# Optimization experiments

Hardware: AMD Instinct MI355X
Metric: run time of the kernel (lower is better)

The kernel has to match this reference:

```python
import jax, jax.numpy as jnp
import numpy as np

DIM = 512
DEPTH = 4
E = 2 ** DEPTH          # 16 experts
HID = 4 * DIM           # mult = 4
B, S = 8, 4096


def setup_inputs() -> dict:
    key = jax.random.key(0)
    ks = jax.random.split(key, 7)
    sc_in = 1.0 / np.sqrt(DIM)
    sc_hid = 1.0 / np.sqrt(HID)
    return {
        "x": jax.random.normal(ks[0], (B, S, DIM), jnp.float32),
        "Wr": jax.random.normal(ks[1], (E - 1, DIM), jnp.float32) * sc_in,
        "br": jax.random.normal(ks[2], (E - 1,), jnp.float32) * 0.01,
        "W1": jax.random.normal(ks[3], (E, DIM, HID), jnp.float32) * sc_in,
        "b1": jax.random.normal(ks[4], (E, HID), jnp.float32) * 0.01,
        "W2": jax.random.normal(ks[5], (E, HID, DIM), jnp.float32) * sc_hid,
        "b2": jax.random.normal(ks[6], (E, DIM), jnp.float32) * 0.01,
    }


def _fff_forward(x, Wr, br, W1, b1, W2, b2):
    Bb, Ss, D = x.shape
    E_ = W1.shape[0]
    depth = int(np.log2(E_))
    xf = x.reshape(-1, D)                      # [N, D]
    N = xf.shape[0]

    # Hard binary-tree routing (inference path of the torch module).
    leaf = jnp.zeros((N,), jnp.int32)
    for d in range(depth):
        off = 2 ** d - 1
        cnt = 2 ** d
        # logits for all routers at this tree level: [N, cnt]
        logits = xf @ Wr[off:off + cnt].T + br[off:off + cnt]
        sel = jnp.take_along_axis(logits, leaf[:, None], axis=1)[:, 0]
        leaf = leaf * 2 + (sel > 0).astype(jnp.int32)

    onehot = jax.nn.one_hot(leaf, E_, dtype=xf.dtype)  # [N, E]

    # Dense weighted-sum dispatch: scan over the (small, fixed) expert axis,
    # accumulating masked expert outputs. Peak extra memory is one [N, HID]
    # activation at a time.
    def body(acc, params):
        w1, bb1, w2, bb2, m = params            # m: [N]
        h = jax.nn.gelu(xf @ w1 + bb1, approximate=False)  # exact GELU (torch nn.GELU)
        y = h @ w2 + bb2
        return acc + m[:, None] * y, None

    out, _ = jax.lax.scan(body, jnp.zeros_like(xf), (W1, b1, W2, b2, onehot.T))
    return out.reshape(Bb, Ss, D)


def reference(x, Wr, br, W1, b1, W2, b2):
    return _fff_forward(x, Wr, br, W1, b1, W2, b2)
```

## Files before the change

kernel.cpp:

```cpp
#include <hip/hip_runtime.h>
#include <math.h>

#define NTOK   32768
#define DMODEL 512
#define HIDDEN 2048
#define NEXP   16
#define TM     256
#define MAXT   144
#define PADN   (MAXT * TM)
#define CPAD   16

typedef short bf16x8 __attribute__((ext_vector_type(8)));
typedef float f32x4  __attribute__((ext_vector_type(4)));

__device__ __forceinline__ short f2bf(float f) {
  union { float f; unsigned int u; } v; v.f = f;
  unsigned int r = v.u + 0x7FFFu + ((v.u >> 16) & 1u);
  return (short)(r >> 16);
}

__device__ __forceinline__ void gload_lds16(const void* g, void* l) {
  __builtin_amdgcn_global_load_lds(
      (const __attribute__((address_space(1))) void*)g,
      (__attribute__((address_space(3))) void*)l, 16, 0, 0);
}

__device__ __forceinline__ float gelu_f(float v) {
  const float u = v * (0.7978845608f + 0.0356774081f * v * v);
  const float au = fabsf(u);
  const float z = __expf(-2.0f * au);
  float T = (1.0f - z) / (1.0f + z);
  T = copysignf(T, u);
  return 0.5f * v * (1.0f + T);
}

__global__ void init_kernel(int* counts, int* cursors) {
  counts[threadIdx.x] = 0; cursors[threadIdx.x] = 0;
}

__global__ __launch_bounds__(256) void route_kernel(
    const float* __restrict__ x, const float* __restrict__ Wr,
    const float* __restrict__ br, short* __restrict__ xb,
    int* __restrict__ leafArr) {
  const int w = threadIdx.x >> 6, l = threadIdx.x & 63;
  const int tok = blockIdx.x * 4 + w;
  const float4* xr = (const float4*)(x + (size_t)tok * DMODEL);
  float4 a0 = xr[l * 2], a1 = xr[l * 2 + 1];

  union { bf16x8 v; short s[8]; } u;
  u.s[0] = f2bf(a0.x); u.s[1] = f2bf(a0.y); u.s[2] = f2bf(a0.z); u.s[3] = f2bf(a0.w);
  u.s[4] = f2bf(a1.x); u.s[5] = f2bf(a1.y); u.s[6] = f2bf(a1.z); u.s[7] = f2bf(a1.w);
  *((bf16x8*)(xb + (size_t)tok * DMODEL) + l) = u.v;

  int leaf = 0;
  for (int d = 0; d < 4; ++d) {
    const int node = (1 << d) - 1 + leaf;
    const float4* wr4 = (const float4*)(Wr + (size_t)node * DMODEL);
    float4 b0 = wr4[l * 2], b1v = wr4[l * 2 + 1];
    double s = (double)a0.x * (double)b0.x + (double)a0.y * (double)b0.y +
               (double)a0.z * (double)b0.z + (double)a0.w * (double)b0.w +
               (double)a1.x * (double)b1v.x + (double)a1.y * (double)b1v.y +
               (double)a1.z * (double)b1v.z + (double)a1.w * (double)b1v.w;
    for (int off = 32; off; off >>= 1) s += __shfl_xor(s, off);
    double sel = s + (double)br[node];
    leaf = leaf * 2 + (sel > 0.0 ? 1 : 0);
  }
  if (l == 0) leafArr[tok] = leaf;
}

__global__ __launch_bounds__(256) void count_kernel(
    const int* __restrict__ leafArr, int* __restrict__ counts,
    int* __restrict__ idx) {
  __shared__ int lcnt[NEXP];
  const int tid = threadIdx.x;
  if (tid < NEXP) lcnt[tid] = 0;
  __syncthreads();
  const int tok = blockIdx.x * 256 + tid;
  atomicAdd(&lcnt[leafArr[tok]], 1);
  __syncthreads();
  if (tid < NEXP && lcnt[tid]) atomicAdd(&counts[tid * CPAD], lcnt[tid]);
  for (int i = blockIdx.x * 256 + tid; i < PADN; i += gridDim.x * 256) idx[i] = 0;
}

__global__ void scan_kernel(const int* __restrict__ counts, int* poff, int* ntiles,
                            int* texp, int* tval) {
  if (threadIdx.x == 0) {
    int po = 0, nt = 0;
    for (int e = 0; e < NEXP; ++e) {
      poff[e] = po;
      const int c = counts[e * CPAD];
      const int t = (c + TM - 1) >> 8;
      for (int i = 0; i < t; ++i) {
        texp[nt] = e;
        int v = c - i * TM; if (v > TM) v = TM;
        tval[nt] = v;
        ++nt;
      }
      po += t << 8;
    }
    poff[NEXP] = po;
    *ntiles = nt;
  }
}

__global__ __launch_bounds__(256) void scatter_kernel(
    const int* __restrict__ leafArr, const int* __restrict__ poff,
    int* cursors, int* __restrict__ idx) {
  __shared__ int lcnt[NEXP], lbase[NEXP];
  const int tid = threadIdx.x;
  if (tid < NEXP) lcnt[tid] = 0;
  __syncthreads();
  const int tok = blockIdx.x * 256 + tid;
  const int e = leafArr[tok];
  const int r = atomicAdd(&lcnt[e], 1);
  __syncthreads();
  if (tid < NEXP) lbase[tid] = lcnt[tid] ? atomicAdd(&cursors[tid * CPAD], lcnt[tid]) : 0;
  __syncthreads();
  idx[poff[e] + lbase[e] + r] = tok;
}

__global__ void tconv_kernel(const float* __restrict__ src, short* __restrict__ dst,
                             int R, int C) {
  __shared__ float tile[32][33];
  const int tx = threadIdx.x, ty = threadIdx.y;
  const int c0 = blockIdx.x * 32, r0 = blockIdx.y * 32;
  const size_t eoff = (size_t)blockIdx.z * R * C;
  for (int i = 0; i < 4; ++i)
    tile[ty + i * 8][tx] = src[eoff + (size_t)(r0 + ty + i * 8) * C + c0 + tx];
  __syncthreads();
  for (int i = 0; i < 4; ++i)
    dst[eoff + (size_t)(c0 + ty + i * 8) * R + r0 + tx] = f2bf(tile[tx][ty + i * 8]);
}


#define STA(pn, ko)                                                            \
  { _Pragma("unroll") for (int j = 0; j < 4; ++j)                              \
      gload_lds16(aSrc[j] + (ko), lds + ((pn) << 14) + j * 4096 + w * 512); }

#define STB(pn, ko)                                                            \
  { _Pragma("unroll") for (int j = 0; j < 4; ++j)                              \
      gload_lds16(bSrc[j] + (ko), lds + 32768 + ((pn) << 14) + j * 4096 + w * 512); }

#define PHASE(mh, ki, STAGE, POST)                                             \
  {                                                                            \
    bf16x8 af[4];                                                              \
    const int sw_ = ((((ki) << 2) + q) ^ (cc & 7)) << 3;                       \
    _Pragma("unroll")                                                          \
    for (int m2 = 0; m2 < 4; ++m2)                                             \
      af[m2] = *(const bf16x8*)(Ab + (wr + ((mh) * 4 + m2) * 16 + cc) * 64 + sw_); \
    if ((mh) == 0) {                                                           \
      _Pragma("unroll")                                                        \
      for (int ni = 0; ni < 4; ++ni)                                           \
        bfv[ni] = *(const bf16x8*)(Bb + (wc + ni * 16 + cc) * 64 + sw_);       \
    }                                                                          \
    STAGE                                                                      \
    __builtin_amdgcn_s_barrier();                                              \
    __builtin_amdgcn_s_setprio(1);                                             \
    _Pragma("unroll")                                                          \
    for (int m2 = 0; m2 < 4; ++m2) {                                           \
      _Pragma("unroll")                                                        \
      for (int ni = 0; ni < 4; ++ni)                                           \
        acc[(mh) * 4 + m2][ni] = __builtin_amdgcn_mfma_f32_16x16x32_bf16(      \
            af[m2], bfv[ni], acc[(mh) * 4 + m2][ni], 0, 0, 0);                 \
    }                                                                          \
    __builtin_amdgcn_s_setprio(0);                                             \
    POST                                                                       \
    __builtin_amdgcn_s_barrier();                                              \
  }

__global__ __launch_bounds__(512, 2) void gemm1_kernel(
    const short* __restrict__ Xb, const short* __restrict__ W1T,
    const float* __restrict__ b1, const int* __restrict__ idx,
    const int* __restrict__ texp, const int* __restrict__ ntiles,
    short* __restrict__ H, int g0) {
  __shared__ short lds[65536];
  const int nb = gridDim.x, bid = blockIdx.x;
  int swz = bid;
  if ((nb & 7) == 0) { const int cpx = nb >> 3; swz = (bid & 7) * cpx + (bid >> 3); }
  const int lt = swz >> 3, cb = swz & 7;
  const int t = g0 + lt;
  if (t >= *ntiles) return;
  const int e = texp[t];
  const int c0 = cb * 256;

  const int tid = threadIdx.x, w = tid >> 6, lane = tid & 63;
  const int q = lane >> 4, cc = lane & 15;
  const int wr = (w >> 2) * 128, wc = (w & 3) * 64;
  const int srow = lane >> 3;
  const int skel = ((lane & 7) ^ srow) * 8;

  const short* aSrc[4]; const short* bSrc[4];
#pragma unroll
  for (int j = 0; j < 4; ++j) {
    const int r = j * 64 + w * 8 + srow;
    const int gt = idx[t * TM + r];
    aSrc[j] = Xb + (size_t)gt * DMODEL + skel;
    bSrc[j] = W1T + ((size_t)e * HIDDEN + c0 + r) * DMODEL + skel;
  }

  f32x4 acc[8][4];
  const f32x4 zero = {0.f, 0.f, 0.f, 0.f};
#pragma unroll
  for (int mi = 0; mi < 8; ++mi)
#pragma unroll
    for (int ni = 0; ni < 4; ++ni) acc[mi][ni] = zero;
  bf16x8 bfv[4];

  STA(0, 0) STB(0, 0)
  asm volatile("s_waitcnt vmcnt(0)" ::: "memory");
  __builtin_amdgcn_s_barrier();

  for (int kt = 0; kt < DMODEL / 64; ++kt) {
    const short* Ab = lds + ((kt & 1) << 14);
    const short* Bb = lds + 32768 + ((kt & 1) << 14);
    const int pn = (kt & 1) ^ 1;
    const int ko = (kt + 1) << 6;
    const bool pre = kt < DMODEL / 64 - 1;
    PHASE(0, 0, if (pre) STA(pn, ko), )
    PHASE(1, 0, if (pre) STB(pn, ko), )
    PHASE(0, 1, , )
    PHASE(1, 1, , asm volatile("s_waitcnt vmcnt(0)" ::: "memory");)
  }

  short* Cs = lds;
#pragma unroll
  for (int ni = 0; ni < 4; ++ni) {
    const int col = wc + ni * 16 + cc;
    const float bv = b1[e * HIDDEN + c0 + col];
#pragma unroll
    for (int mi = 0; mi < 8; ++mi) {
#pragma unroll
      for (int r = 0; r < 4; ++r) {
        const int row = wr + mi * 16 + q * 4 + r;
        const float v = gelu_f(acc[mi][ni][r] + bv);
        Cs[row * 256 + ((((col >> 3) ^ (row & 15)) << 3) | (col & 7))] = f2bf(v);
      }
    }
  }
  __syncthreads();
#pragma unroll
  for (int it = 0; it < 16; ++it) {
    const int lin = tid + it * 512;
    const int row = lin >> 5;
    const int s = lin & 31;
    const bf16x8 vv = *(const bf16x8*)(Cs + row * 256 + s * 8);
    const int ch = s ^ (row & 15);
    *(bf16x8*)(H + ((size_t)lt * TM + row) * HIDDEN + c0 + (ch << 3)) = vv;
  }
}

__global__ __launch_bounds__(512, 2) void gemm2_kernel(
    const short* __restrict__ H, const short* __restrict__ W2T,
    const float* __restrict__ b2, const int* __restrict__ idx,
    const int* __restrict__ texp, const int* __restrict__ tval,
    const int* __restrict__ ntiles, float* __restrict__ out, int g0) {
  __shared__ short lds[65536];
  const int nb = gridDim.x, bid = blockIdx.x;
  int swz = bid;
  if ((nb & 7) == 0) { const int cpx = nb >> 3; swz = (bid & 7) * cpx + (bid >> 3); }
  const int lt = swz >> 1, cb = swz & 1;
  const int t = g0 + lt;
  if (t >= *ntiles) return;
  const int e = texp[t];
  const int c0 = cb * 256;

  const int tid = threadIdx.x, w = tid >> 6, lane = tid & 63;
  const int q = lane >> 4, cc = lane & 15;
  const int wr = (w >> 2) * 128, wc = (w & 3) * 64;
  const int srow = lane >> 3;
  const int skel = ((lane & 7) ^ srow) * 8;

  const short* aSrc[4]; const short* bSrc[4];
#pragma unroll
  for (int j = 0; j < 4; ++j) {
    const int r = j * 64 + w * 8 + srow;
    aSrc[j] = H + ((size_t)lt * TM + r) * HIDDEN + skel;
    bSrc[j] = W2T + ((size_t)e * DMODEL + c0 + r) * HIDDEN + skel;
  }

  f32x4 acc[8][4];
  const f32x4 zero = {0.f, 0.f, 0.f, 0.f};
#pragma unroll
  for (int mi = 0; mi < 8; ++mi)
#pragma unroll
    for (int ni = 0; ni < 4; ++ni) acc[mi][ni] = zero;
  bf16x8 bfv[4];

  STA(0, 0) STB(0, 0)
  asm volatile("s_waitcnt vmcnt(0)" ::: "memory");
  __builtin_amdgcn_s_barrier();

  for (int kt = 0; kt < HIDDEN / 64; ++kt) {
    const short* Ab = lds + ((kt & 1) << 14);
    const short* Bb = lds + 32768 + ((kt & 1) << 14);
    const int pn = (kt & 1) ^ 1;
    const int ko = (kt + 1) << 6;
    const bool pre = kt < HIDDEN / 64 - 1;
    PHASE(0, 0, if (pre) STA(pn, ko), )
    PHASE(1, 0, if (pre) STB(pn, ko), )
    PHASE(0, 1, , )
    PHASE(1, 1, , asm volatile("s_waitcnt vmcnt(0)" ::: "memory");)
  }

  const int nv = tval[t];
#pragma unroll
  for (int ni = 0; ni < 4; ++ni) {
    const int col = c0 + wc + ni * 16 + cc;
    const float bv = b2[e * DMODEL + col];
#pragma unroll
    for (int mi = 0; mi < 8; ++mi) {
#pragma unroll
      for (int r = 0; r < 4; ++r) {
        const int row = wr + mi * 16 + q * 4 + r;
        if (row < nv) {
          const int tok = idx[t * TM + row];
          out[(size_t)tok * DMODEL + col] = acc[mi][ni][r] + bv;
        }
      }
    }
  }
}

extern "C" void kernel_launch(void* const* d_in, const int* in_sizes, int n_in,
                              void* d_out, int out_size, void* d_ws, size_t ws_size,
                              hipStream_t stream) {
  (void)in_sizes; (void)n_in; (void)out_size;
  const float* x  = (const float*)d_in[0];
  const float* Wr = (const float*)d_in[1];
  const float* br = (const float*)d_in[2];
  const float* W1 = (const float*)d_in[3];
  const float* b1 = (const float*)d_in[4];
  const float* W2 = (const float*)d_in[5];
  const float* b2 = (const float*)d_in[6];
  float* out = (float*)d_out;
  char* ws = (char*)d_ws;

  int* counts  = (int*)(ws + 0);
  int* cursors = (int*)(ws + 1024);
  int* poff    = (int*)(ws + 2048);
  int* ntiles  = (int*)(ws + 2304);
  int* texp    = (int*)(ws + 4096);
  int* tval    = (int*)(ws + 8192);
  int* leafA   = (int*)(ws + 16384);
  int* idx     = (int*)(ws + 16384 + 131072);

  const size_t MB32 = 33554432ull;
  short* Xb  = (short*)(ws + (1ull << 20));
  short* W1T = (short*)(ws + (1ull << 20) + MB32);
  short* W2T = (short*)(ws + (1ull << 20) + 2 * MB32);
  short* Hb  = (short*)(ws + (1ull << 20) + 3 * MB32);
  const size_t o_h = (1ull << 20) + 3 * MB32;
  const size_t perTile = (size_t)TM * HIDDEN * sizeof(short);

  int TPG = MAXT;
  if (ws_size < o_h + (size_t)MAXT * perTile) {
    size_t avail = ws_size > o_h ? ws_size - o_h : 0;
    TPG = (int)(avail / perTile);
    TPG &= ~3;
    if (TPG < 4) TPG = 4;
  }
  const int ngroups = (MAXT + TPG - 1) / TPG;

  hipLaunchKernelGGL(init_kernel,    dim3(1),          dim3(256),   0, stream, counts, cursors);
  hipLaunchKernelGGL(route_kernel,   dim3(NTOK / 4),   dim3(256),   0, stream, x, Wr, br, Xb, leafA);
  hipLaunchKernelGGL(count_kernel,   dim3(NTOK / 256), dim3(256),   0, stream, leafA, counts, idx);
  hipLaunchKernelGGL(scan_kernel,    dim3(1),          dim3(64),    0, stream, counts, poff, ntiles, texp, tval);
  hipLaunchKernelGGL(scatter_kernel, dim3(NTOK / 256), dim3(256),   0, stream, leafA, poff, cursors, idx);
  hipLaunchKernelGGL(tconv_kernel,   dim3(64, 16, 16), dim3(32, 8), 0, stream, W1, W1T, DMODEL, HIDDEN);
  hipLaunchKernelGGL(tconv_kernel,   dim3(16, 64, 16), dim3(32, 8), 0, stream, W2, W2T, HIDDEN, DMODEL);

  for (int g = 0; g < ngroups; ++g) {
    hipLaunchKernelGGL(gemm1_kernel, dim3(TPG * 8), dim3(512), 0, stream,
                       Xb, W1T, b1, idx, texp, ntiles, Hb, g * TPG);
    hipLaunchKernelGGL(gemm2_kernel, dim3(TPG * 2), dim3(512), 0, stream,
                       Hb, W2T, b2, idx, texp, tval, ntiles, out, g * TPG);
  }
}
```

Before: 572.6 us.

## Prefetch weight tiles two k-steps ahead with partial vmcnt waits

Replaces the one-stage prefetch loop in both expert GEMMs with a shared KLOOP macro. Activation (A) tiles are still loaded one k-step ahead, split into two half-loads across the first two phases. Weight (B) tiles are now loaded two k-steps ahead into the current buffer once it has been consumed. The end-of-step wait becomes vmcnt(4) instead of vmcnt(0), so one B prefetch stays in flight across the barrier and more global-load latency is hidden behind MFMA work. The cost is more complex ordering that depends on every wave having finished reading the B buffer before it is refilled.

```diff
diff --git a/kernel.cpp b/kernel.cpp
--- a/kernel.cpp
+++ b/kernel.cpp
@@ -133,11 +133,11 @@
 }
 
 
-#define STA(pn, ko)                                                            \
-  { _Pragma("unroll") for (int j = 0; j < 4; ++j)                              \
+#define STA2(pn, ko, J0)                                                       \
+  { _Pragma("unroll") for (int j = (J0); j < (J0) + 2; ++j)                    \
       gload_lds16(aSrc[j] + (ko), lds + ((pn) << 14) + j * 4096 + w * 512); }
 
-#define STB(pn, ko)                                                            \
+#define STB4(pn, ko)                                                           \
   { _Pragma("unroll") for (int j = 0; j < 4; ++j)                              \
       gload_lds16(bSrc[j] + (ko), lds + 32768 + ((pn) << 14) + j * 4096 + w * 512); }
 
@@ -168,6 +168,24 @@
     __builtin_amdgcn_s_barrier();                                              \
   }
 
+#define KLOOP(NKT)                                                             \
+  STA2(0, 0, 0) STA2(0, 0, 2) STB4(0, 0) STB4(1, 64)                           \
+  asm volatile("s_waitcnt vmcnt(4)" ::: "memory");                             \
+  __builtin_amdgcn_s_barrier();                                                \
+  for (int kt = 0; kt < (NKT); ++kt) {                                         \
+    const int cur = kt & 1, pn = cur ^ 1;                                      \
+    const short* Ab = lds + (cur << 14);                                       \
+    const short* Bb = lds + 32768 + (cur << 14);                               \
+    const int ko1 = (kt + 1) << 6, ko2 = (kt + 2) << 6;                        \
+    const bool p1ok = kt + 1 < (NKT), p2ok = kt + 2 < (NKT);                   \
+    PHASE(0, 0, if (p1ok) STA2(pn, ko1, 0), )                                  \
+    PHASE(1, 0, if (p1ok) STA2(pn, ko1, 2), )                                  \
+    PHASE(0, 1, , )                                                            \
+    PHASE(1, 1, if (p2ok) STB4(cur, ko2),                                      \
+          if (p2ok) { asm volatile("s_waitcnt vmcnt(4)" ::: "memory"); }       \
+          else      { asm volatile("s_waitcnt vmcnt(0)" ::: "memory"); } )     \
+  }
+
 __global__ __launch_bounds__(512, 2) void gemm1_kernel(
     const short* __restrict__ Xb, const short* __restrict__ W1T,
     const float* __restrict__ b1, const int* __restrict__ idx,
@@ -206,21 +224,7 @@
     for (int ni = 0; ni < 4; ++ni) acc[mi][ni] = zero;
   bf16x8 bfv[4];
 
-  STA(0, 0) STB(0, 0)
-  asm volatile("s_waitcnt vmcnt(0)" ::: "memory");
-  __builtin_amdgcn_s_barrier();
-
-  for (int kt = 0; kt < DMODEL / 64; ++kt) {
-    const short* Ab = lds + ((kt & 1) << 14);
-    const short* Bb = lds + 32768 + ((kt & 1) << 14);
-    const int pn = (kt & 1) ^ 1;
-    const int ko = (kt + 1) << 6;
-    const bool pre = kt < DMODEL / 64 - 1;
-    PHASE(0, 0, if (pre) STA(pn, ko), )
-    PHASE(1, 0, if (pre) STB(pn, ko), )
-    PHASE(0, 1, , )
-    PHASE(1, 1, , asm volatile("s_waitcnt vmcnt(0)" ::: "memory");)
-  }
+  KLOOP(DMODEL / 64)
 
   short* Cs = lds;
 #pragma unroll
@@ -286,21 +290,7 @@
     for (int ni = 0; ni < 4; ++ni) acc[mi][ni] = zero;
   bf16x8 bfv[4];
 
-  STA(0, 0) STB(0, 0)
-  asm volatile("s_waitcnt vmcnt(0)" ::: "memory");
-  __builtin_amdgcn_s_barrier();
-
-  for (int kt = 0; kt < HIDDEN / 64; ++kt) {
-    const short* Ab = lds + ((kt & 1) << 14);
-    const short* Bb = lds + 32768 + ((kt & 1) << 14);
-    const int pn = (kt & 1) ^ 1;
-    const int ko = (kt + 1) << 6;
-    const bool pre = kt < HIDDEN / 64 - 1;
-    PHASE(0, 0, if (pre) STA(pn, ko), )
-    PHASE(1, 0, if (pre) STB(pn, ko), )
-    PHASE(0, 1, , )
-    PHASE(1, 1, , asm volatile("s_waitcnt vmcnt(0)" ::: "memory");)
-  }
+  KLOOP(HIDDEN / 64)
 
   const int nv = tval[t];
 #pragma unroll
```

Result: no change. 565.0 us (-1.3%).
